# Kernel optimization log

Measured on AMD Instinct MI355X. Metric: run time of the kernel, lower is better.

Reference implementation:

```python
import jax, jax.numpy as jnp
import numpy as np

N_GRAPHS = 32
N_NODES = 2048          # nodes per graph == lstm1 input_size
N_TOTAL = N_GRAPHS * N_NODES
N_EDGES = 1048576
HEADS = 8
GAT_OUT = 12            # per-head GAT output dim (== num_features)
OUT_CH = 9
NEG_SLOPE = 0.2
BN_EPS = 1e-5


def setup_inputs() -> dict:
    key = jax.random.key(0)
    ks = jax.random.split(key, 20)
    inp = {}
    inp['x'] = jax.random.normal(ks[0], (N_TOTAL, GAT_OUT), jnp.float32)
    inp['edge_index'] = jax.random.randint(ks[1], (2, N_EDGES), 0, N_TOTAL, jnp.int64)
    inp['W_gat'] = jax.random.normal(ks[2], (GAT_OUT, HEADS * GAT_OUT), jnp.float32) * 0.3
    inp['a_src'] = jax.random.normal(ks[3], (HEADS, GAT_OUT), jnp.float32) * 0.3
    inp['a_dst'] = jax.random.normal(ks[4], (HEADS, GAT_OUT), jnp.float32) * 0.3
    inp['gat_bias'] = jax.random.normal(ks[5], (GAT_OUT,), jnp.float32) * 0.1
    inp['bn_gamma'] = jax.random.uniform(ks[6], (GAT_OUT,), jnp.float32, 0.5, 1.5)
    inp['bn_beta'] = jax.random.normal(ks[7], (GAT_OUT,), jnp.float32) * 0.1
    inp['bn_mean'] = jax.random.normal(ks[8], (GAT_OUT,), jnp.float32) * 0.1
    inp['bn_var'] = jax.random.uniform(ks[9], (GAT_OUT,), jnp.float32, 0.5, 1.5)
    inp['w_ih1'] = jax.random.normal(ks[10], (4 * 32, N_NODES), jnp.float32) / np.sqrt(N_NODES)
    inp['w_hh1'] = jax.random.normal(ks[11], (4 * 32, 32), jnp.float32) / np.sqrt(32)
    inp['b_ih1'] = jnp.zeros((4 * 32,), jnp.float32)
    inp['b_hh1'] = jnp.zeros((4 * 32,), jnp.float32)
    inp['w_ih2'] = jax.random.normal(ks[12], (4 * 128, 32), jnp.float32) / np.sqrt(32)
    inp['w_hh2'] = jax.random.normal(ks[13], (4 * 128, 128), jnp.float32) / np.sqrt(128)
    inp['b_ih2'] = jnp.zeros((4 * 128,), jnp.float32)
    inp['b_hh2'] = jnp.zeros((4 * 128,), jnp.float32)
    inp['lin_w'] = jax.random.normal(ks[14], (N_NODES, 128), jnp.float32) / np.sqrt(128)
    inp['lin_b'] = jax.random.normal(ks[15], (N_NODES,), jnp.float32) * 0.1
    return inp


def _gat(x, edge_index, W, a_src, a_dst, bias):
    # PyG GATConv, heads=HEADS, out=GAT_OUT, concat=False (mean over heads), eval mode.
    N = x.shape[0]
    xp = (x @ W).reshape(N, HEADS, GAT_OUT)               # [N,H,C]
    loops = jnp.arange(N, dtype=edge_index.dtype)
    src = jnp.concatenate([edge_index[0], loops])
    dst = jnp.concatenate([edge_index[1], loops])
    asrc = jnp.einsum('nhc,hc->nh', xp, a_src)            # [N,H]
    adst = jnp.einsum('nhc,hc->nh', xp, a_dst)
    e = jax.nn.leaky_relu(asrc[src] + adst[dst], NEG_SLOPE)  # [E,H]
    m = jax.ops.segment_max(e, dst, num_segments=N)
    e = jnp.exp(e - m[dst])
    denom = jax.ops.segment_sum(e, dst, num_segments=N)
    alpha = e / (denom[dst] + 1e-16)
    msg = xp[src] * alpha[:, :, None]                     # [E,H,C]
    out = jax.ops.segment_sum(msg, dst, num_segments=N)   # [N,H,C]
    return out.mean(axis=1) + bias                        # concat=False -> head mean


def _lstm(x_seq, w_ih, w_hh, b_ih, b_hh):
    # x_seq: [T,B,I]; PyTorch gate order i,f,g,o.
    Hh = w_hh.shape[1]
    B = x_seq.shape[1]
    bias = b_ih + b_hh

    def step(carry, xt):
        h, c = carry
        gates = xt @ w_ih.T + h @ w_hh.T + bias
        i, f, g, o = jnp.split(gates, 4, axis=-1)
        c = jax.nn.sigmoid(f) * c + jax.nn.sigmoid(i) * jnp.tanh(g)
        h = jax.nn.sigmoid(o) * jnp.tanh(c)
        return (h, c), h

    init = (jnp.zeros((B, Hh), x_seq.dtype), jnp.zeros((B, Hh), x_seq.dtype))
    _, hs = jax.lax.scan(step, init, x_seq)
    return hs


def reference(x, edge_index, W_gat, a_src, a_dst, gat_bias,
              bn_gamma, bn_beta, bn_mean, bn_var,
              w_ih1, w_hh1, b_ih1, b_hh1,
              w_ih2, w_hh2, b_ih2, b_hh2,
              lin_w, lin_b):
    h = _gat(x, edge_index, W_gat, a_src, a_dst, gat_bias)          # [N,12]
    h = (h - bn_mean) / jnp.sqrt(bn_var + BN_EPS) * bn_gamma + bn_beta
    # dropout inactive in eval mode
    h = jax.nn.log_softmax(h, axis=1)
    h = h.reshape(N_GRAPHS, N_NODES, GAT_OUT)
    h = jnp.moveaxis(h, 2, 0)                                       # [T=12,B,n]
    h = _lstm(h, w_ih1, w_hh1, b_ih1, b_hh1)                        # [12,B,32]
    h = _lstm(h, w_ih2, w_hh2, b_ih2, b_hh2)                        # [12,B,128]
    h = h @ lin_w.T + lin_b                                         # [12,B,n]
    h = h[-OUT_CH:]                                                 # [9,B,n]
    h = jnp.moveaxis(h, 0, 2)                                       # [B,n,9]
    return h.reshape(N_GRAPHS * N_NODES, OUT_CH)
```

## Files before the change

kernel.cpp:

```cpp
#include <hip/hip_runtime.h>
#include <math.h>

#define N_EDGES_C 1048576
#define N_TOTAL_C 65536

typedef _Float16 h2v __attribute__((ext_vector_type(2)));
typedef int i4v __attribute__((ext_vector_type(4)));

#if defined(__has_builtin)
#if __has_builtin(__builtin_amdgcn_fdot2)
#define HAS_FDOT2 1
#endif
#if __has_builtin(__builtin_amdgcn_rcpf)
#define HAS_RCPF 1
#endif
#endif

__device__ __forceinline__ float fdot2(h2v a, h2v b, float c) {
#ifdef HAS_FDOT2
    return __builtin_amdgcn_fdot2(a, b, c, false);
#else
    return c + (float)a.x * (float)b.x + (float)a.y * (float)b.y;
#endif
}

__device__ __forceinline__ float fast_rcp(float x) {
#ifdef HAS_RCPF
    return __builtin_amdgcn_rcpf(x);
#else
    return 1.0f / x;
#endif
}
__device__ __forceinline__ float sigf(float x){ return fast_rcp(1.0f + __expf(-x)); }
__device__ __forceinline__ float tanh_fast(float x){ return fmaf(2.0f, fast_rcp(1.0f + __expf(-2.0f*x)), -1.0f); }
__device__ __forceinline__ float lrelu(float x){ return (x>=0.f)? x : 0.2f*x; }


__global__ void prep_kernel(const float* __restrict__ x, const float* __restrict__ Wg,
                            const float* __restrict__ a_src, const float* __restrict__ a_dst,
                            _Float16* __restrict__ xpp)
{
    int tid = threadIdx.x;
    __shared__ float Ws[12*96];
    __shared__ float as_s[96], ad_s[96];
    for (int i = tid; i < 1152; i += 256) Ws[i] = Wg[i];
    if (tid < 96) { as_s[tid] = a_src[tid]; ad_s[tid] = a_dst[tid]; }
    __syncthreads();
    int h = tid >> 5;
    int n = blockIdx.x * 32 + (tid & 31);
    const float4* xv = (const float4*)(x + (size_t)n * 12);
    float4 v0 = xv[0], v1 = xv[1], v2 = xv[2];
    float xr[12] = {v0.x,v0.y,v0.z,v0.w, v1.x,v1.y,v1.z,v1.w, v2.x,v2.y,v2.z,v2.w};
    float xp_[12];
    #pragma unroll
    for (int c = 0; c < 12; c++) {
        float acc = 0.f;
        #pragma unroll
        for (int k = 0; k < 12; k++) acc += xr[k] * Ws[k*96 + h*12 + c];
        xp_[c] = acc;
    }
    float sa = 0.f, sd = 0.f;
    #pragma unroll
    for (int c = 0; c < 12; c++) { sa += xp_[c]*as_s[h*12+c]; sd += xp_[c]*ad_s[h*12+c]; }
    union { _Float16 hh[16]; float ff[8]; float4 f4[2]; } s;
    #pragma unroll
    for (int c = 0; c < 12; c++) s.hh[c] = (_Float16)xp_[c];
    s.ff[6] = sa;
    s.ff[7] = sd;
    float4* o = (float4*)(xpp + ((size_t)h * 65536 + n) * 16);
    o[0] = s.f4[0];
    o[1] = s.f4[1];
}

__global__ __launch_bounds__(256)
void edge_hist(const int* __restrict__ ei, unsigned* __restrict__ cnt,
               unsigned* __restrict__ rank8)
{
    __shared__ unsigned hist[16384];
    int tid = threadIdx.x;
    int slice = blockIdx.x;
    for (int i = tid; i < 16384; i += 256) hist[i] = 0;
    __syncthreads();
    const i4v* dst4 = (const i4v*)(ei + N_EDGES_C) + slice*2048;
    for (int i = tid; i < 2048; i += 256) {
        i4v d = __builtin_nontemporal_load(&dst4[i]);
        int dd[4] = {d.x, d.y, d.z, d.w};
        unsigned packed = 0;
        #pragma unroll
        for (int j = 0; j < 4; j++) {
            int dj = dd[j];
            unsigned sh = (unsigned)(dj & 3) << 3;
            unsigned old = atomicAdd(&hist[dj >> 2], 1u << sh);
            packed |= ((old >> sh) & 0xffu) << (j*8);
        }
        __builtin_nontemporal_store(packed, &rank8[slice*2048 + i]);
    }
    __syncthreads();
    unsigned* cg = cnt + (size_t)slice*16384;
    for (int i = tid; i < 16384; i += 256) cg[i] = hist[i];
}

__global__ __launch_bounds__(128)
void slice_prefix(unsigned* __restrict__ cnt, int* __restrict__ deg)
{
    int w = blockIdx.x*128 + threadIdx.x;
    unsigned run = 0;
    unsigned* base = cnt + w;
    #pragma unroll 1
    for (int s = 0; s < 128; s += 32) {
        unsigned v[32];
        #pragma unroll
        for (int k = 0; k < 32; k++) v[k] = base[(size_t)(s+k)*16384];
        #pragma unroll
        for (int k = 0; k < 32; k++) {
            base[(size_t)(s+k)*16384] = run;
            run += v[k];
        }
    }
    ((int4*)deg)[w] = make_int4((int)(run & 255u), (int)((run >> 8) & 255u),
                                (int)((run >> 16) & 255u), (int)(run >> 24));
}

__global__ void scan_build(const int* __restrict__ deg, int* __restrict__ rowptr)
{
    __shared__ int sums[1024];
    int tid = threadIdx.x;
    int4 v[16];
    const int4* deg4 = (const int4*)deg;
    #pragma unroll
    for (int j = 0; j < 16; j++) v[j] = deg4[tid*16 + j];
    int s = 0;
    #pragma unroll
    for (int j = 0; j < 16; j++) s += v[j].x + v[j].y + v[j].z + v[j].w;
    sums[tid] = s;
    __syncthreads();
    for (int off = 1; off < 1024; off <<= 1) {
        int t = 0;
        if (tid >= off) t = sums[tid - off];
        __syncthreads();
        if (tid >= off) sums[tid] += t;
        __syncthreads();
    }
    int run = sums[tid] - s;
    int4* rp4 = (int4*)rowptr;
    #pragma unroll
    for (int j = 0; j < 16; j++) {
        int4 r;
        r.x = run; run += v[j].x;
        r.y = run; run += v[j].y;
        r.z = run; run += v[j].z;
        r.w = run; run += v[j].w;
        rp4[tid*16 + j] = r;
    }
    if (tid == 1023) rowptr[65536] = run;
}

__global__ __launch_bounds__(256)
void edge_scatter(const int* __restrict__ ei, const unsigned* __restrict__ rank8,
                  const unsigned* __restrict__ cnt, const int* __restrict__ rowptr,
                  int* __restrict__ csr)
{
    __shared__ unsigned pos_s[2048];
    __shared__ int src_s[2048];
    int slice = blockIdx.x >> 2;
    int quar  = blockIdx.x & 3;
    int base = slice*2048 + quar*512;
    const i4v* dst4 = (const i4v*)(ei + N_EDGES_C);
    const i4v* src4 = (const i4v*)ei;
    const unsigned* cslice = cnt + (size_t)slice*16384;
    for (int i = threadIdx.x; i < 512; i += 256) {
        int idx = base + i;
        i4v d = __builtin_nontemporal_load(&dst4[idx]);
        i4v s = __builtin_nontemporal_load(&src4[idx]);
        unsigned r = __builtin_nontemporal_load(&rank8[idx]);
        int dd[4] = {d.x, d.y, d.z, d.w};
        int ss[4] = {s.x, s.y, s.z, s.w};
        #pragma unroll
        for (int j = 0; j < 4; j++) {
            int dj = dd[j];
            unsigned word = cslice[dj >> 2];
            int so = (int)((word >> ((unsigned)(dj & 3) << 3)) & 0xffu);
            int rk = (int)((r >> (j*8)) & 0xffu);
            unsigned pos = (unsigned)(rowptr[dj] + so + rk);
            pos_s[i*4 + j] = pos | ((unsigned)(dj >> 13) << 24);
            src_s[i*4 + j] = ss[j];
        }
    }
    __syncthreads();
    #pragma unroll 1
    for (unsigned g = 0; g < 8; g++) {
        for (int e = threadIdx.x; e < 2048; e += 256) {
            unsigned pw = pos_s[e];
            if ((pw >> 24) == g) csr[pw & 0xFFFFFFu] = src_s[e];
        }
    }
}

__global__ __launch_bounds__(256)
void gat_aggregate(const _Float16* __restrict__ xpp,
                   const int* __restrict__ rowptr, const int* __restrict__ csr_src,
                   float* __restrict__ partial)
{
    int head = blockIdx.x & 7;
    int n = (blockIdx.x >> 3) * 256 + threadIdx.x;
    const _Float16* xh = xpp + (size_t)head * (65536 * 16);

    float acc[12];
    float adst_n, d;
    {
        const float4* p = (const float4*)(xh + (size_t)n * 16);
        float4 f0 = p[0], f1 = p[1];
        adst_n = f1.w;
        float w = __expf(lrelu(f1.z + adst_n));
        d = w;
        h2v c0 = __builtin_bit_cast(h2v, f0.x), c1 = __builtin_bit_cast(h2v, f0.y);
        h2v c2 = __builtin_bit_cast(h2v, f0.z), c3 = __builtin_bit_cast(h2v, f0.w);
        h2v c4 = __builtin_bit_cast(h2v, f1.x), c5 = __builtin_bit_cast(h2v, f1.y);
        acc[0]=w*(float)c0.x; acc[1]=w*(float)c0.y; acc[2]=w*(float)c1.x; acc[3]=w*(float)c1.y;
        acc[4]=w*(float)c2.x; acc[5]=w*(float)c2.y; acc[6]=w*(float)c3.x; acc[7]=w*(float)c3.y;
        acc[8]=w*(float)c4.x; acc[9]=w*(float)c4.y; acc[10]=w*(float)c5.x; acc[11]=w*(float)c5.y;
    }

    auto accum = [&](float4 f0, float4 f1) {
        float w = __expf(lrelu(f1.z + adst_n));
        d += w;
        h2v c0 = __builtin_bit_cast(h2v, f0.x), c1 = __builtin_bit_cast(h2v, f0.y);
        h2v c2 = __builtin_bit_cast(h2v, f0.z), c3 = __builtin_bit_cast(h2v, f0.w);
        h2v c4 = __builtin_bit_cast(h2v, f1.x), c5 = __builtin_bit_cast(h2v, f1.y);
        acc[0]+=w*(float)c0.x; acc[1]+=w*(float)c0.y; acc[2]+=w*(float)c1.x; acc[3]+=w*(float)c1.y;
        acc[4]+=w*(float)c2.x; acc[5]+=w*(float)c2.y; acc[6]+=w*(float)c3.x; acc[7]+=w*(float)c3.y;
        acc[8]+=w*(float)c4.x; acc[9]+=w*(float)c4.y; acc[10]+=w*(float)c5.x; acc[11]+=w*(float)c5.y;
    };

    int beg = rowptr[n], end = rowptr[n+1];
    int i = beg;
    for (; i + 4 <= end; i += 4) {
        int s0 = csr_src[i+0];
        int s1 = csr_src[i+1];
        int s2 = csr_src[i+2];
        int s3 = csr_src[i+3];
        const float4* p0 = (const float4*)(xh + (size_t)s0*16);
        const float4* p1 = (const float4*)(xh + (size_t)s1*16);
        const float4* p2 = (const float4*)(xh + (size_t)s2*16);
        const float4* p3 = (const float4*)(xh + (size_t)s3*16);
        float4 a0 = p0[0], b0 = p0[1];
        float4 a1 = p1[0], b1 = p1[1];
        float4 a2 = p2[0], b2 = p2[1];
        float4 a3 = p3[0], b3 = p3[1];
        accum(a0, b0);
        accum(a1, b1);
        accum(a2, b2);
        accum(a3, b3);
    }
    for (; i < end; i++) {
        int src = csr_src[i];
        const float4* p = (const float4*)(xh + (size_t)src*16);
        float4 f0 = p[0], f1 = p[1];
        accum(f0, f1);
    }

    float inv = 1.0f / (d + 1e-16f);
    #pragma unroll
    for (int c = 0; c < 12; c++)
        __builtin_nontemporal_store(acc[c] * inv,
                                    &partial[((size_t)c*8 + head)*65536 + n]);
}

__global__ __launch_bounds__(256)
void gat_reduce(const float* __restrict__ partial,
                const float* __restrict__ gat_bias, const float* __restrict__ bn_gamma,
                const float* __restrict__ bn_beta, const float* __restrict__ bn_mean,
                const float* __restrict__ bn_var, float* __restrict__ seq)
{
    int n = blockIdx.x * 256 + threadIdx.x;
    float vals[12];
    float mx = -1e30f;
    #pragma unroll
    for (int c = 0; c < 12; c++) {
        const float* b = partial + (size_t)c*8*65536 + n;
        float p0 = __builtin_nontemporal_load(b + 0*65536);
        float p1 = __builtin_nontemporal_load(b + 1*65536);
        float p2 = __builtin_nontemporal_load(b + 2*65536);
        float p3 = __builtin_nontemporal_load(b + 3*65536);
        float p4 = __builtin_nontemporal_load(b + 4*65536);
        float p5 = __builtin_nontemporal_load(b + 5*65536);
        float p6 = __builtin_nontemporal_load(b + 6*65536);
        float p7 = __builtin_nontemporal_load(b + 7*65536);
        float v = ((p0 + p1) + (p2 + p3)) + ((p4 + p5) + (p6 + p7));
        float res = v * 0.125f;
        float t = res + gat_bias[c];
        t = (t - bn_mean[c]) * rsqrtf(bn_var[c] + 1e-5f) * bn_gamma[c] + bn_beta[c];
        vals[c] = t;
        mx = fmaxf(mx, t);
    }
    float sum = 0.f;
    #pragma unroll
    for (int c = 0; c < 12; c++) sum += __expf(vals[c] - mx);
    float lse = __logf(sum) + mx;
    #pragma unroll
    for (int c = 0; c < 12; c++)
        __builtin_nontemporal_store(vals[c] - lse, &seq[(size_t)c * N_TOTAL_C + n]);
}

__global__ void gemm_x1(const float* __restrict__ A, const float* __restrict__ B,
                        float* __restrict__ C)
{
    __shared__ float As[32][33], Bs[32][33];
    const int K = 2048, N = 128;
    int tid = threadIdx.x;
    int tx = tid & 31, ty = tid >> 5;
    int bm = blockIdx.x * 32, bn = blockIdx.y * 32;
    int kbase = blockIdx.z * 128;
    float acc[4] = {0.f,0.f,0.f,0.f};
    for (int kk = 0; kk < 128; kk += 32) {
        int k0 = kbase + kk;
        #pragma unroll
        for (int i = 0; i < 4; i++) {
            int r = ty + i*8;
            As[r][tx] = A[(size_t)(bm + r) * K + k0 + tx];
            Bs[r][tx] = B[(size_t)(bn + r) * K + k0 + tx];
        }
        __syncthreads();
        #pragma unroll
        for (int k = 0; k < 32; k++) {
            float bv = Bs[tx][k];
            #pragma unroll
            for (int i = 0; i < 4; i++) acc[i] += As[ty + i*8][k] * bv;
        }
        __syncthreads();
    }
    #pragma unroll
    for (int i = 0; i < 4; i++)
        atomicAdd(&C[(size_t)(bm + ty + i*8) * N + bn + tx], acc[i]);
}

__global__ __launch_bounds__(512)
void lstm_fused(const float* __restrict__ X1, const float* __restrict__ w_hh1,
                const float* __restrict__ b_ih1, const float* __restrict__ b_hh1,
                const float* __restrict__ w_ih2, const float* __restrict__ w_hh2,
                const float* __restrict__ b_ih2, const float* __restrict__ b_hh2,
                float* __restrict__ H2)
{
    __shared__ float whh1[128*33];
    __shared__ float b1s[128];
    __shared__ float h1[32], c1[32];
    __shared__ __align__(16) _Float16 h1s[32];
    __shared__ __align__(16) _Float16 h2s[128];
    __shared__ float c2[128];
    __shared__ float g1s[128], g2s[512];
    int tid = threadIdx.x;
    int b = blockIdx.x;

    h2v whh[64];
    {
        const float2* wh = (const float2*)(w_hh2 + (size_t)tid * 128);
        #pragma unroll
        for (int k = 0; k < 64; k++) {
            float2 v = wh[k];
            h2v t; t.x = (_Float16)v.x; t.y = (_Float16)v.y;
            whh[k] = t;
        }
    }
    h2v wih[16];
    {
        const float2* wi = (const float2*)(w_ih2 + (size_t)tid * 32);
        #pragma unroll
        for (int k = 0; k < 16; k++) {
            float2 v = wi[k];
            h2v t; t.x = (_Float16)v.x; t.y = (_Float16)v.y;
            wih[k] = t;
        }
    }
    float b2 = b_ih2[tid] + b_hh2[tid];

    for (int i = tid; i < 128*32; i += 512) whh1[(i >> 5)*33 + (i & 31)] = w_hh1[i];
    if (tid < 128) b1s[tid] = b_ih1[tid] + b_hh1[tid];
    if (tid < 32)  { h1[tid] = 0.f; c1[tid] = 0.f; h1s[tid] = (_Float16)0.f; }
    if (tid < 128) { c2[tid] = 0.f; h2s[tid] = (_Float16)0.f; }

    float xv = 0.f;
    if (tid < 128) xv = X1[((size_t)0*32 + b)*128 + tid];
    __syncthreads();

    for (int t = 0; t < 12; t++) {
        float xv_next = 0.f;
        if (t < 11 && tid < 128) xv_next = X1[((size_t)(t+1)*32 + b)*128 + tid];

        float p0 = b2, p1 = 0.f, p2 = 0.f, p3 = 0.f;
        #pragma unroll
        for (int j = 0; j < 16; j++) {
            float4 f = ((const float4*)h2s)[j];
            p0 = fdot2(__builtin_bit_cast(h2v, f.x), whh[j*4+0], p0);
            p1 = fdot2(__builtin_bit_cast(h2v, f.y), whh[j*4+1], p1);
            p2 = fdot2(__builtin_bit_cast(h2v, f.z), whh[j*4+2], p2);
            p3 = fdot2(__builtin_bit_cast(h2v, f.w), whh[j*4+3], p3);
        }
        float acc2 = (p0 + p1) + (p2 + p3);

        if (tid < 128) {
            const float* wr = &whh1[tid * 33];
            float acc = xv + b1s[tid];
            #pragma unroll
            for (int k = 0; k < 32; k++) acc += h1[k] * wr[k];
            g1s[tid] = acc;
        }
        __syncthreads();
        if (tid < 32) {
            float ig = sigf(g1s[tid]), fg = sigf(g1s[32+tid]);
            float gg = tanh_fast(g1s[64+tid]), og = sigf(g1s[96+tid]);
            float cn = fg * c1[tid] + ig * gg;
            c1[tid] = cn;
            float hn = og * tanh_fast(cn);
            h1[tid] = hn;
            h1s[tid] = (_Float16)hn;
        }
        __syncthreads();
        {
            float q0 = 0.f, q1 = 0.f, q2 = 0.f, q3 = 0.f;
            #pragma unroll
            for (int j = 0; j < 4; j++) {
                float4 f = ((const float4*)h1s)[j];
                q0 = fdot2(__builtin_bit_cast(h2v, f.x), wih[j*4+0], q0);
                q1 = fdot2(__builtin_bit_cast(h2v, f.y), wih[j*4+1], q1);
                q2 = fdot2(__builtin_bit_cast(h2v, f.z), wih[j*4+2], q2);
                q3 = fdot2(__builtin_bit_cast(h2v, f.w), wih[j*4+3], q3);
            }
            g2s[tid] = acc2 + (q0 + q1) + (q2 + q3);
        }
        __syncthreads();
        if (tid < 128) {
            float ig = sigf(g2s[tid]), fg = sigf(g2s[128+tid]);
            float gg = tanh_fast(g2s[256+tid]), og = sigf(g2s[384+tid]);
            float cn = fg * c2[tid] + ig * gg;
            c2[tid] = cn;
            float hn = og * tanh_fast(cn);
            h2s[tid] = (_Float16)hn;
            if (t >= 3) H2[((size_t)t*32 + b)*128 + tid] = hn;
        }
        __syncthreads();
        xv = xv_next;
    }
}

__global__ void gemm_out(const float* __restrict__ A, const float* __restrict__ B,
                         const float* __restrict__ bias, float* __restrict__ out)
{
    __shared__ float As[32][33], Bs[32][33];
    const int K = 128;
    int tid = threadIdx.x;
    int tx = tid & 31, ty = tid >> 5;
    int bm = blockIdx.x * 32, bn = blockIdx.y * 32;
    float acc[4] = {0.f,0.f,0.f,0.f};
    for (int k0 = 0; k0 < K; k0 += 32) {
        #pragma unroll
        for (int i = 0; i < 4; i++) {
            int r = ty + i*8;
            As[r][tx] = A[(size_t)(bm + r) * K + k0 + tx];
            Bs[r][tx] = B[(size_t)(bn + r) * K + k0 + tx];
        }
        __syncthreads();
        #pragma unroll
        for (int kk = 0; kk < 32; kk++) {
            float bv = Bs[tx][kk];
            #pragma unroll
            for (int i = 0; i < 4; i++) acc[i] += As[ty + i*8][kk] * bv;
        }
        __syncthreads();
    }
    int j = blockIdx.x;
    int nn = bn + tx;
    float bv = bias[nn];
    #pragma unroll
    for (int i = 0; i < 4; i++) {
        int bb = ty + i*8;
        out[((size_t)bb * 2048 + nn) * 9 + j] = acc[i] + bv;
    }
}

extern "C" void kernel_launch(void* const* d_in, const int* in_sizes, int n_in,
                              void* d_out, int out_size, void* d_ws, size_t ws_size,
                              hipStream_t stream)
{
    const float* x        = (const float*)d_in[0];
    const int*   ei       = (const int*)  d_in[1];
    const float* W_gat    = (const float*)d_in[2];
    const float* a_src    = (const float*)d_in[3];
    const float* a_dst    = (const float*)d_in[4];
    const float* gat_bias = (const float*)d_in[5];
    const float* bn_gamma = (const float*)d_in[6];
    const float* bn_beta  = (const float*)d_in[7];
    const float* bn_mean  = (const float*)d_in[8];
    const float* bn_var   = (const float*)d_in[9];
    const float* w_ih1    = (const float*)d_in[10];
    const float* w_hh1    = (const float*)d_in[11];
    const float* b_ih1    = (const float*)d_in[12];
    const float* b_hh1    = (const float*)d_in[13];
    const float* w_ih2    = (const float*)d_in[14];
    const float* w_hh2    = (const float*)d_in[15];
    const float* b_ih2    = (const float*)d_in[16];
    const float* b_hh2    = (const float*)d_in[17];
    const float* lin_w    = (const float*)d_in[18];
    const float* lin_b    = (const float*)d_in[19];
    float* out = (float*)d_out;

    float* ws = (float*)d_ws;
    _Float16* xpp = (_Float16*)ws;
    float* seq  = ws + 4194304;
    float* X1   = seq + 786432;
    float* H2   = X1  + 49152;
    int* rowptr = (int*)(H2 + 49152);
    int* deg    = rowptr + 65544;
    unsigned* cnt = (unsigned*)(deg + 65536);
    unsigned* rank8 = cnt + 2097152;
    int* csr    = (int*)(rank8 + 262144);
    float* partial = (float*)(csr + 1048576);

    hipMemsetAsync(X1, 0, 49152 * sizeof(float), stream);
    prep_kernel <<<2048, 256, 0, stream>>>(x, W_gat, a_src, a_dst, xpp);
    edge_hist   <<<128, 256, 0, stream>>>(ei, cnt, rank8);
    slice_prefix<<<128, 128, 0, stream>>>(cnt, deg);
    scan_build  <<<1, 1024, 0, stream>>>(deg, rowptr);
    edge_scatter<<<512, 256, 0, stream>>>(ei, rank8, cnt, rowptr, csr);
    gat_aggregate<<<2048, 256, 0, stream>>>(xpp, rowptr, csr, partial);
    gat_reduce  <<<256, 256, 0, stream>>>(partial, gat_bias, bn_gamma, bn_beta,
                                          bn_mean, bn_var, seq);
    gemm_x1<<<dim3(12, 4, 16), 256, 0, stream>>>(seq, w_ih1, X1);
    lstm_fused<<<32, 512, 0, stream>>>(X1, w_hh1, b_ih1, b_hh1, w_ih2, w_hh2, b_ih2, b_hh2, H2);
    gemm_out<<<dim3(9, 64), 256, 0, stream>>>(H2 + 96*128, lin_w, lin_b, out);
}
```

Baseline: 296.6 us.

## Interleave head pairs in xpp layout so each gather fetches two heads

Projected node features are stored with two heads interleaved per 64-byte record (four slices of head pairs) instead of one 32-byte record per head. The aggregation kernel now processes two heads per thread, so each edge's CSR index load and row-pointer read serve two heads and each gather fetches a contiguous 64-byte line. This halves the grid and the number of CSR traversals. In exchange, per-thread registers double for the accumulators, the edge-loop unroll drops from 4 to 2, and CSR index loads become nontemporal.

After: 307.6 us. 3.7% more time.

```diff
diff --git a/kernel.cpp b/kernel.cpp
--- a/kernel.cpp
+++ b/kernel.cpp
@@ -46,8 +46,9 @@
     for (int i = tid; i < 1152; i += 256) Ws[i] = Wg[i];
     if (tid < 96) { as_s[tid] = a_src[tid]; ad_s[tid] = a_dst[tid]; }
     __syncthreads();
-    int h = tid >> 5;
-    int n = blockIdx.x * 32 + (tid & 31);
+    int gid = blockIdx.x * 256 + tid;
+    int n = gid >> 3;
+    int h = gid & 7;
     const float4* xv = (const float4*)(x + (size_t)n * 12);
     float4 v0 = xv[0], v1 = xv[1], v2 = xv[2];
     float xr[12] = {v0.x,v0.y,v0.z,v0.w, v1.x,v1.y,v1.z,v1.w, v2.x,v2.y,v2.z,v2.w};
@@ -67,7 +68,8 @@
     for (int c = 0; c < 12; c++) s.hh[c] = (_Float16)xp_[c];
     s.ff[6] = sa;
     s.ff[7] = sd;
-    float4* o = (float4*)(xpp + ((size_t)h * 65536 + n) * 16);
+    int slice = h >> 1, hl = h & 1;
+    float4* o = (float4*)(xpp + (size_t)slice * (65536*32) + (size_t)n * 32 + hl * 16);
     o[0] = s.f4[0];
     o[1] = s.f4[1];
 }
@@ -201,69 +203,70 @@
                    const int* __restrict__ rowptr, const int* __restrict__ csr_src,
                    float* __restrict__ partial)
 {
-    int head = blockIdx.x & 7;
-    int n = (blockIdx.x >> 3) * 256 + threadIdx.x;
-    const _Float16* xh = xpp + (size_t)head * (65536 * 16);
-
-    float acc[12];
-    float adst_n, d;
-    {
-        const float4* p = (const float4*)(xh + (size_t)n * 16);
-        float4 f0 = p[0], f1 = p[1];
-        adst_n = f1.w;
+    int slice = blockIdx.x & 3;
+    int n = (blockIdx.x >> 2) * 256 + threadIdx.x;
+    const _Float16* xh = xpp + (size_t)slice * (65536*32);
+
+    float accA[12], accB[12];
+    float adstA, adstB, dA, dB;
+
+    auto accumH = [](float4 f0, float4 f1, float adst_n, float* acc, float& d, bool init) {
         float w = __expf(lrelu(f1.z + adst_n));
-        d = w;
+        d = init ? w : d + w;
         h2v c0 = __builtin_bit_cast(h2v, f0.x), c1 = __builtin_bit_cast(h2v, f0.y);
         h2v c2 = __builtin_bit_cast(h2v, f0.z), c3 = __builtin_bit_cast(h2v, f0.w);
         h2v c4 = __builtin_bit_cast(h2v, f1.x), c5 = __builtin_bit_cast(h2v, f1.y);
-        acc[0]=w*(float)c0.x; acc[1]=w*(float)c0.y; acc[2]=w*(float)c1.x; acc[3]=w*(float)c1.y;
-        acc[4]=w*(float)c2.x; acc[5]=w*(float)c2.y; acc[6]=w*(float)c3.x; acc[7]=w*(float)c3.y;
-        acc[8]=w*(float)c4.x; acc[9]=w*(float)c4.y; acc[10]=w*(float)c5.x; acc[11]=w*(float)c5.y;
-    }
-
-    auto accum = [&](float4 f0, float4 f1) {
-        float w = __expf(lrelu(f1.z + adst_n));
-        d += w;
-        h2v c0 = __builtin_bit_cast(h2v, f0.x), c1 = __builtin_bit_cast(h2v, f0.y);
-        h2v c2 = __builtin_bit_cast(h2v, f0.z), c3 = __builtin_bit_cast(h2v, f0.w);
-        h2v c4 = __builtin_bit_cast(h2v, f1.x), c5 = __builtin_bit_cast(h2v, f1.y);
-        acc[0]+=w*(float)c0.x; acc[1]+=w*(float)c0.y; acc[2]+=w*(float)c1.x; acc[3]+=w*(float)c1.y;
-        acc[4]+=w*(float)c2.x; acc[5]+=w*(float)c2.y; acc[6]+=w*(float)c3.x; acc[7]+=w*(float)c3.y;
-        acc[8]+=w*(float)c4.x; acc[9]+=w*(float)c4.y; acc[10]+=w*(float)c5.x; acc[11]+=w*(float)c5.y;
+        if (init) {
+            acc[0]=w*(float)c0.x; acc[1]=w*(float)c0.y; acc[2]=w*(float)c1.x; acc[3]=w*(float)c1.y;
+            acc[4]=w*(float)c2.x; acc[5]=w*(float)c2.y; acc[6]=w*(float)c3.x; acc[7]=w*(float)c3.y;
+            acc[8]=w*(float)c4.x; acc[9]=w*(float)c4.y; acc[10]=w*(float)c5.x; acc[11]=w*(float)c5.y;
+        } else {
+            acc[0]+=w*(float)c0.x; acc[1]+=w*(float)c0.y; acc[2]+=w*(float)c1.x; acc[3]+=w*(float)c1.y;
+            acc[4]+=w*(float)c2.x; acc[5]+=w*(float)c2.y; acc[6]+=w*(float)c3.x; acc[7]+=w*(float)c3.y;
+            acc[8]+=w*(float)c4.x; acc[9]+=w*(float)c4.y; acc[10]+=w*(float)c5.x; acc[11]+=w*(float)c5.y;
+        }
     };
+
+    {
+        const float4* p = (const float4*)(xh + (size_t)n * 32);
+        float4 f0 = p[0], f1 = p[1], f2 = p[2], f3 = p[3];
+        adstA = f1.w; adstB = f3.w;
+        accumH(f0, f1, adstA, accA, dA, true);
+        accumH(f2, f3, adstB, accB, dB, true);
+    }
 
     int beg = rowptr[n], end = rowptr[n+1];
     int i = beg;
-    for (; i + 4 <= end; i += 4) {
-        int s0 = csr_src[i+0];
-        int s1 = csr_src[i+1];
-        int s2 = csr_src[i+2];
-        int s3 = csr_src[i+3];
-        const float4* p0 = (const float4*)(xh + (size_t)s0*16);
-        const float4* p1 = (const float4*)(xh + (size_t)s1*16);
-        const float4* p2 = (const float4*)(xh + (size_t)s2*16);
-        const float4* p3 = (const float4*)(xh + (size_t)s3*16);
-        float4 a0 = p0[0], b0 = p0[1];
-        float4 a1 = p1[0], b1 = p1[1];
-        float4 a2 = p2[0], b2 = p2[1];
-        float4 a3 = p3[0], b3 = p3[1];
-        accum(a0, b0);
-        accum(a1, b1);
-        accum(a2, b2);
-        accum(a3, b3);
+    for (; i + 2 <= end; i += 2) {
+        int s0 = __builtin_nontemporal_load(&csr_src[i+0]);
+        int s1 = __builtin_nontemporal_load(&csr_src[i+1]);
+        const float4* p0 = (const float4*)(xh + (size_t)s0*32);
+        const float4* p1 = (const float4*)(xh + (size_t)s1*32);
+        float4 a0 = p0[0], a1 = p0[1], a2 = p0[2], a3 = p0[3];
+        float4 b0 = p1[0], b1 = p1[1], b2 = p1[2], b3 = p1[3];
+        accumH(a0, a1, adstA, accA, dA, false);
+        accumH(a2, a3, adstB, accB, dB, false);
+        accumH(b0, b1, adstA, accA, dA, false);
+        accumH(b2, b3, adstB, accB, dB, false);
     }
     for (; i < end; i++) {
-        int src = csr_src[i];
-        const float4* p = (const float4*)(xh + (size_t)src*16);
-        float4 f0 = p[0], f1 = p[1];
-        accum(f0, f1);
-    }
-
-    float inv = 1.0f / (d + 1e-16f);
-    #pragma unroll
-    for (int c = 0; c < 12; c++)
-        __builtin_nontemporal_store(acc[c] * inv,
-                                    &partial[((size_t)c*8 + head)*65536 + n]);
+        int src = __builtin_nontemporal_load(&csr_src[i]);
+        const float4* p = (const float4*)(xh + (size_t)src*32);
+        float4 f0 = p[0], f1 = p[1], f2 = p[2], f3 = p[3];
+        accumH(f0, f1, adstA, accA, dA, false);
+        accumH(f2, f3, adstB, accB, dB, false);
+    }
+
+    float invA = 1.0f / (dA + 1e-16f);
+    float invB = 1.0f / (dB + 1e-16f);
+    int headA = slice*2, headB = slice*2 + 1;
+    #pragma unroll
+    for (int c = 0; c < 12; c++) {
+        __builtin_nontemporal_store(accA[c] * invA,
+                                    &partial[((size_t)c*8 + headA)*65536 + n]);
+        __builtin_nontemporal_store(accB[c] * invB,
+                                    &partial[((size_t)c*8 + headB)*65536 + n]);
+    }
 }
 
 __global__ __launch_bounds__(256)
@@ -521,7 +524,7 @@
     slice_prefix<<<128, 128, 0, stream>>>(cnt, deg);
     scan_build  <<<1, 1024, 0, stream>>>(deg, rowptr);
     edge_scatter<<<512, 256, 0, stream>>>(ei, rank8, cnt, rowptr, csr);
-    gat_aggregate<<<2048, 256, 0, stream>>>(xpp, rowptr, csr, partial);
+    gat_aggregate<<<1024, 256, 0, stream>>>(xpp, rowptr, csr, partial);
     gat_reduce  <<<256, 256, 0, stream>>>(partial, gat_bias, bn_gamma, bn_beta,
                                           bn_mean, bn_var, seq);
     gemm_x1<<<dim3(12, 4, 16), 256, 0, stream>>>(seq, w_ih1, X1);
```
